# Performance work log

Hardware: AMD Instinct MI355X
Metric: run time of the kernel (lower is better)

The kernel has to match this reference:

```python
import jax, jax.numpy as jnp
import numpy as np

M, N, K = 8, 4096, 16  # samples, simplices (Laplacian dim), n_filters


def setup_inputs() -> dict:
    key = jax.random.key(0)
    kx, kl, kw = jax.random.split(key, 3)
    x = jax.random.normal(kx, (M, N, N), dtype=jnp.float32)   # stacked x_list
    L = jax.random.normal(kl, (N, N), dtype=jnp.float32)      # Laplacian
    W = 0.01 * jax.random.normal(kw, (K, N), dtype=jnp.float32)  # filter weights
    return {"x": x, "L": L, "W": W}


def reference(x, L, W):
    # Original math per sample x_b [n,n]:
    #   Lx[i,j]   = (L @ x_b[i])[j] = sum_m L[j,m] x_b[i,m]
    #   weighted  = diag(w_k) @ Lx          -> row i scaled by w_k[i]
    #   filt_out  = act(sum_j weighted[i,j]) = act(w_k[i] * sum_j Lx[i,j])
    # sum_j Lx[i,j] = x_b[i] . colsum(L), so the dense [n,n] diag matmul
    # collapses to a matvec + broadcasted scale (same math, fused form).
    col = jnp.sum(L, axis=0)                       # [n]
    s = jnp.einsum('bim,m->bi', x, col)            # [M, n]
    # sum over filters of tanh(w_k * s)
    out = jnp.sum(jnp.tanh(W[None, :, :] * s[:, None, :]), axis=1)  # [M, n]
    return out
```

## Files before the change

### kernel.cpp

```cpp
#include <hip/hip_runtime.h>

#define NN 4096
#define MM 8
#define KK 16

typedef float v4f __attribute__((ext_vector_type(4)));

#define WS_COL     0
#define WS_PARTIAL 4096
#define WS_WT      (4096 + 64 * 4096)

__global__ void __launch_bounds__(256) colsum_stage1(const float* __restrict__ L,
                                                     float* __restrict__ ws) {
    const int t  = threadIdx.x;
    const int m4 = blockIdx.x * 64 + (t & 63);
    const int r0 = blockIdx.y * 64 + (t >> 6) * 16;
    const v4f* __restrict__ L4 = reinterpret_cast<const v4f*>(L);
    v4f acc = {0.f, 0.f, 0.f, 0.f};
#pragma unroll
    for (int j = 0; j < 16; ++j) {
        acc += __builtin_nontemporal_load(&L4[(size_t)(r0 + j) * (NN / 4) + m4]);
    }
    __shared__ v4f red[256];
    red[t] = acc;
    __syncthreads();
    if (t < 64) {
        const v4f s = red[t] + red[t + 64] + red[t + 128] + red[t + 192];
        reinterpret_cast<v4f*>(ws + WS_PARTIAL)[blockIdx.y * (NN / 4) + blockIdx.x * 64 + t] = s;
    }
}

__global__ void __launch_bounds__(256) colsum_stage2(const float* __restrict__ W,
                                                     float* __restrict__ ws) {
    const int b = blockIdx.x;
    const int t = threadIdx.x;
    if (b < 4) {
        const int slot = b * 256 + t;
        const v4f* __restrict__ p4 = reinterpret_cast<const v4f*>(ws + WS_PARTIAL);
        v4f acc = {0.f, 0.f, 0.f, 0.f};
#pragma unroll 8
        for (int j = 0; j < 64; ++j) {
            acc += p4[j * (NN / 4) + slot];
        }
        reinterpret_cast<v4f*>(ws + WS_COL)[slot] = acc;
    } else {
        float* __restrict__ Wt = ws + WS_WT;
        for (int o = (b - 4) * 256 + t; o < NN * KK; o += 12 * 256) {
            const int i = o >> 4;
            const int k = o & 15;
            Wt[o] = W[k * NN + i];
        }
    }
}

__global__ void __launch_bounds__(256) conv_kernel(const float* __restrict__ x,
                                                   const float* __restrict__ ws,
                                                   float* __restrict__ out) {
    const int wave = threadIdx.x >> 6;
    const int lane = threadIdx.x & 63;
    const int row  = blockIdx.x * 4 + wave;
    const int i    = row & (NN - 1);

    const v4f* __restrict__ xr = reinterpret_cast<const v4f*>(x) + (size_t)row * (NN / 4);
    const v4f* __restrict__ cv = reinterpret_cast<const v4f*>(ws + WS_COL);

    float acc = 0.f;
#pragma unroll
    for (int it = 0; it < NN / 4 / 64; ++it) {
        const v4f a = __builtin_nontemporal_load(&xr[it * 64 + lane]);
        const v4f c = cv[it * 64 + lane];
        const v4f p = a * c;
        acc += p.x + p.y + p.z + p.w;
    }

#pragma unroll
    for (int off = 32; off >= 1; off >>= 1)
        acc += __shfl_xor(acc, off, 64);

    float r = 0.f;
    if (lane < KK) r = tanhf((ws + WS_WT)[i * KK + lane] * acc);
#pragma unroll
    for (int off = 8; off >= 1; off >>= 1)
        r += __shfl_down(r, off, 64);

    if (lane == 0) out[row] = r;
}

extern "C" void kernel_launch(void* const* d_in, const int* in_sizes, int n_in,
                              void* d_out, int out_size, void* d_ws, size_t ws_size,
                              hipStream_t stream) {
    const float* x = (const float*)d_in[0];
    const float* L = (const float*)d_in[1];
    const float* W = (const float*)d_in[2];
    float* out = (float*)d_out;
    float* ws  = (float*)d_ws;

    colsum_stage1<<<dim3(16, 64), 256, 0, stream>>>(L, ws);
    colsum_stage2<<<16, 256, 0, stream>>>(W, ws);
    conv_kernel<<<(MM * NN) / 4, 256, 0, stream>>>(x, ws, out);
}
```

Measured before the change: 100.9 us.

## Stage colsum in LDS, use fast tanh, move W transpose into stage one

The W transpose moves into an extra row of blocks in the first colsum kernel, so stage two only reduces the partial sums. The conv kernel copies the colsum vector into LDS once per block and reads it from there instead of global memory, and its loop unroll drops from full to 4. tanhf is replaced by an exp/reciprocal approximation, which costs a little accuracy. The conv kernel is bound by streaming x (8x4096x4096 floats), so these edits mostly trim launch and latency overhead around that stream.

```diff
diff --git a/kernel.cpp b/kernel.cpp
--- a/kernel.cpp
+++ b/kernel.cpp
@@ -11,8 +11,18 @@
 #define WS_WT      (4096 + 64 * 4096)
 
 __global__ void __launch_bounds__(256) colsum_stage1(const float* __restrict__ L,
+                                                     const float* __restrict__ W,
                                                      float* __restrict__ ws) {
-    const int t  = threadIdx.x;
+    const int t = threadIdx.x;
+    if (blockIdx.y == 64) {
+        float* __restrict__ Wt = ws + WS_WT;
+        for (int o = blockIdx.x * 256 + t; o < NN * KK; o += 16 * 256) {
+            const int i = o >> 4;
+            const int k = o & 15;
+            Wt[o] = W[k * NN + i];
+        }
+        return;
+    }
     const int m4 = blockIdx.x * 64 + (t & 63);
     const int r0 = blockIdx.y * 64 + (t >> 6) * 16;
     const v4f* __restrict__ L4 = reinterpret_cast<const v4f*>(L);
@@ -30,45 +40,46 @@
     }
 }
 
-__global__ void __launch_bounds__(256) colsum_stage2(const float* __restrict__ W,
-                                                     float* __restrict__ ws) {
-    const int b = blockIdx.x;
-    const int t = threadIdx.x;
-    if (b < 4) {
-        const int slot = b * 256 + t;
-        const v4f* __restrict__ p4 = reinterpret_cast<const v4f*>(ws + WS_PARTIAL);
-        v4f acc = {0.f, 0.f, 0.f, 0.f};
+__global__ void __launch_bounds__(256) colsum_stage2(float* __restrict__ ws) {
+    const int slot = blockIdx.x * 256 + threadIdx.x;
+    const v4f* __restrict__ p4 = reinterpret_cast<const v4f*>(ws + WS_PARTIAL);
+    v4f acc = {0.f, 0.f, 0.f, 0.f};
 #pragma unroll 8
-        for (int j = 0; j < 64; ++j) {
-            acc += p4[j * (NN / 4) + slot];
-        }
-        reinterpret_cast<v4f*>(ws + WS_COL)[slot] = acc;
-    } else {
-        float* __restrict__ Wt = ws + WS_WT;
-        for (int o = (b - 4) * 256 + t; o < NN * KK; o += 12 * 256) {
-            const int i = o >> 4;
-            const int k = o & 15;
-            Wt[o] = W[k * NN + i];
-        }
+    for (int j = 0; j < 64; ++j) {
+        acc += p4[j * (NN / 4) + slot];
     }
+    reinterpret_cast<v4f*>(ws + WS_COL)[slot] = acc;
+}
+
+__device__ __forceinline__ float fast_tanh(float a) {
+    const float e = __expf(2.f * fabsf(a));
+    const float t = 1.f - 2.f * __builtin_amdgcn_rcpf(e + 1.f);
+    return copysignf(t, a);
 }
 
 __global__ void __launch_bounds__(256) conv_kernel(const float* __restrict__ x,
                                                    const float* __restrict__ ws,
                                                    float* __restrict__ out) {
-    const int wave = threadIdx.x >> 6;
-    const int lane = threadIdx.x & 63;
+    __shared__ v4f col_lds[NN / 4];
+    const int t = threadIdx.x;
+#pragma unroll
+    for (int j = 0; j < 4; ++j) {
+        col_lds[j * 256 + t] = reinterpret_cast<const v4f*>(ws + WS_COL)[j * 256 + t];
+    }
+    __syncthreads();
+
+    const int wave = t >> 6;
+    const int lane = t & 63;
     const int row  = blockIdx.x * 4 + wave;
     const int i    = row & (NN - 1);
 
     const v4f* __restrict__ xr = reinterpret_cast<const v4f*>(x) + (size_t)row * (NN / 4);
-    const v4f* __restrict__ cv = reinterpret_cast<const v4f*>(ws + WS_COL);
 
     float acc = 0.f;
-#pragma unroll
+#pragma unroll 4
     for (int it = 0; it < NN / 4 / 64; ++it) {
         const v4f a = __builtin_nontemporal_load(&xr[it * 64 + lane]);
-        const v4f c = cv[it * 64 + lane];
+        const v4f c = col_lds[it * 64 + lane];
         const v4f p = a * c;
         acc += p.x + p.y + p.z + p.w;
     }
@@ -78,7 +89,7 @@
         acc += __shfl_xor(acc, off, 64);
 
     float r = 0.f;
-    if (lane < KK) r = tanhf((ws + WS_WT)[i * KK + lane] * acc);
+    if (lane < KK) r = fast_tanh((ws + WS_WT)[i * KK + lane] * acc);
 #pragma unroll
     for (int off = 8; off >= 1; off >>= 1)
         r += __shfl_down(r, off, 64);
@@ -95,7 +106,7 @@
     float* out = (float*)d_out;
     float* ws  = (float*)d_ws;
 
-    colsum_stage1<<<dim3(16, 64), 256, 0, stream>>>(L, ws);
-    colsum_stage2<<<16, 256, 0, stream>>>(W, ws);
+    colsum_stage1<<<dim3(16, 65), 256, 0, stream>>>(L, W, ws);
+    colsum_stage2<<<4, 256, 0, stream>>>(ws);
     conv_kernel<<<(MM * NN) / 4, 256, 0, stream>>>(x, ws, out);
 }
```

Result: no change. 102.3 us (+1.4%).
